# Kernel tuning notes

Hardware: AMD Instinct MI355X
Metric: run time of the kernel (lower is better)

The kernel has to match this reference:

```python
import jax, jax.numpy as jnp
import numpy as np
import math

B, S, SENC, D, H, FF, V = 4, 512, 512, 1024, 16, 4096, 50257
MAX_HOP = 6          # n_layers -> max ACT hops
THRESH = 1.0 - 0.01  # ACT halting threshold
EPS = 1e-12          # LAYER_NORM_EPS
NEG = -1e20          # neginf for fp32 masking
DH = D // H


def _sincos(n_pos, dim):
    # create_position_codes: sin on even dims, cos on odd dims
    pos = np.arange(n_pos, dtype=np.float64)[:, None]
    j = np.arange(dim // 2, dtype=np.float64)[None, :]
    ang = pos / np.power(10000.0, 2.0 * j / dim)
    out = np.zeros((n_pos, dim), dtype=np.float32)
    out[:, 0::2] = np.sin(ang)
    out[:, 1::2] = np.cos(ang)
    return jnp.asarray(out)


def setup_inputs() -> dict:
    key = jax.random.key(0)
    ks = jax.random.split(key, 20)
    def lin_w(k, fan_in, fan_out):
        return (jax.random.normal(k, (fan_in, fan_out), jnp.float32)
                * (1.0 / math.sqrt(fan_in)))
    inp = {
        "tokens": jax.random.randint(ks[0], (B, S), 0, V),
        "encoder_output": jax.random.normal(ks[1], (B, SENC, D), jnp.float32),
        "encoder_mask": jnp.ones((B, SENC), jnp.int32),
        "emb": jax.random.normal(ks[2], (V, D), jnp.float32) * 0.02,
        "sa_qw": lin_w(ks[3], D, D), "sa_qb": jnp.zeros((D,), jnp.float32),
        "sa_kw": lin_w(ks[4], D, D), "sa_kb": jnp.zeros((D,), jnp.float32),
        "sa_vw": lin_w(ks[5], D, D), "sa_vb": jnp.zeros((D,), jnp.float32),
        "sa_ow": lin_w(ks[6], D, D), "sa_ob": jnp.zeros((D,), jnp.float32),
        "ca_qw": lin_w(ks[7], D, D), "ca_qb": jnp.zeros((D,), jnp.float32),
        "ca_kw": lin_w(ks[8], D, D), "ca_kb": jnp.zeros((D,), jnp.float32),
        "ca_vw": lin_w(ks[9], D, D), "ca_vb": jnp.zeros((D,), jnp.float32),
        "ca_ow": lin_w(ks[10], D, D), "ca_ob": jnp.zeros((D,), jnp.float32),
        "ln1_g": jnp.ones((D,), jnp.float32), "ln1_b": jnp.zeros((D,), jnp.float32),
        "ln2_g": jnp.ones((D,), jnp.float32), "ln2_b": jnp.zeros((D,), jnp.float32),
        "ln3_g": jnp.ones((D,), jnp.float32), "ln3_b": jnp.zeros((D,), jnp.float32),
        "ff_w1": lin_w(ks[11], D, FF), "ff_b1": jnp.zeros((FF,), jnp.float32),
        "ff_w2": lin_w(ks[12], FF, D), "ff_b2": jnp.zeros((D,), jnp.float32),
        "act_w": jax.random.normal(ks[13], (D,), jnp.float32) * 0.02,
        "act_b": jnp.ones((), jnp.float32),  # p.bias.data.fill_(1)
    }
    return inp


def _ln(x, g, b):
    m = x.mean(-1, keepdims=True)
    v = ((x - m) ** 2).mean(-1, keepdims=True)
    return (x - m) / jnp.sqrt(v + EPS) * g + b


def _mha(x, kv, maskb, qw, qb, kw, kb, vw, vb, ow, ob):
    Bq, Sq, _ = x.shape
    Sk = kv.shape[1]
    q = (x @ qw + qb).reshape(Bq, Sq, H, DH).transpose(0, 2, 1, 3) / math.sqrt(DH)
    k = (kv @ kw + kb).reshape(Bq, Sk, H, DH).transpose(0, 2, 1, 3)
    v = (kv @ vw + vb).reshape(Bq, Sk, H, DH).transpose(0, 2, 1, 3)
    sc = jnp.einsum('bhqd,bhkd->bhqk', q, k)
    sc = jnp.where(maskb, sc, NEG)
    a = jax.nn.softmax(sc, axis=-1)
    o = jnp.einsum('bhqk,bhkd->bhqd', a, v).transpose(0, 2, 1, 3).reshape(Bq, Sq, D)
    return o @ ow + ob


def reference(tokens, encoder_output, encoder_mask, emb,
              sa_qw, sa_qb, sa_kw, sa_kb, sa_vw, sa_vb, sa_ow, sa_ob,
              ca_qw, ca_qb, ca_kw, ca_kb, ca_vw, ca_vb, ca_ow, ca_ob,
              ln1_g, ln1_b, ln2_g, ln2_b, ln3_g, ln3_b,
              ff_w1, ff_b1, ff_w2, ff_b2, act_w, act_b):
    pos_codes = _sincos(S, D)       # [S, D]
    time_codes = _sincos(MAX_HOP, D)  # [MAX_HOP, D]
    x = emb[tokens] * math.sqrt(D)  # embeddings_scale
    dec_mask = jnp.tril(jnp.ones((S, S), bool))[None, None]          # causal
    enc_maskb = (encoder_mask != 0)[:, None, None, :]                # [B,1,1,Senc]

    def layer(t):
        r = t
        t = _mha(t, t, dec_mask, sa_qw, sa_qb, sa_kw, sa_kb, sa_vw, sa_vb, sa_ow, sa_ob)
        t = _ln(t + r, ln1_g, ln1_b)
        r = t
        t = _mha(t, encoder_output, enc_maskb, ca_qw, ca_qb, ca_kw, ca_kb, ca_vw, ca_vb, ca_ow, ca_ob)
        t = _ln(t + r, ln2_g, ln2_b)
        r = t
        t = jax.nn.relu(t @ ff_w1 + ff_b1) @ ff_w2 + ff_b2
        return _ln(t + r, ln3_g, ln3_b)

    def step(carry, t_idx):
        tensor, prev, hp, rem, nup = carry
        tensor = tensor + pos_codes[None] + time_codes[t_idx][None, None]
        p = jax.nn.sigmoid(tensor @ act_w + act_b)                   # [B,S]
        still = (hp < 1.0).astype(jnp.float32)
        cond = hp + p * still
        new_halted = (cond > THRESH).astype(jnp.float32) * still
        still = (cond <= THRESH).astype(jnp.float32) * still
        hp = hp + p * still
        rem = rem + new_halted * (1.0 - hp)
        hp = hp + new_halted * rem
        nup = nup + still + new_halted
        uw = (p * still + new_halted * rem)[..., None]
        tensor = layer(tensor)
        prev = tensor * uw + prev * (1.0 - uw)
        return (tensor, prev, hp, rem, nup), None

    z = jnp.zeros((B, S), jnp.float32)
    init = (x, jnp.zeros_like(x), z, z, z)
    # Running all MAX_HOP steps is exactly equivalent to the torch while-loop:
    # after a position halts, its update weight is 0 and state is frozen.
    (_, prev, hp, rem, nup), _ = jax.lax.scan(step, init, jnp.arange(MAX_HOP))
    return prev
```

## Files before the change

kernel.cpp:

```cpp
#include <hip/hip_runtime.h>
#include <math.h>

#define BB 4
#define SS 512
#define SE 512
#define DD 1024
#define HH 16
#define FFD 4096
#define NHOP 6

typedef float f32x4 __attribute__((ext_vector_type(4)));
typedef _Float16 h8 __attribute__((ext_vector_type(8)));

#define GLD16(gp, lp)                                                     \
  __builtin_amdgcn_global_load_lds(                                       \
      (const __attribute__((address_space(1))) void*)(gp),                \
      (__attribute__((address_space(3))) void*)(lp), 16, 0, 0)

template <int N>
__device__ __forceinline__ void vwait() {
  if constexpr (N == 0) asm volatile("s_waitcnt vmcnt(0)" ::: "memory");
  else if constexpr (N == 4) asm volatile("s_waitcnt vmcnt(4)" ::: "memory");
  else if constexpr (N == 6) asm volatile("s_waitcnt vmcnt(6)" ::: "memory");
  else if constexpr (N == 8) asm volatile("s_waitcnt vmcnt(8)" ::: "memory");
}

__device__ __forceinline__ float blockSum256(float v, float* s4) {
#pragma unroll
  for (int m = 32; m >= 1; m >>= 1) v += __shfl_xor(v, m);
  __syncthreads();
  if ((threadIdx.x & 63) == 0) s4[threadIdx.x >> 6] = v;
  __syncthreads();
  return s4[0] + s4[1] + s4[2] + s4[3];
}

__device__ __forceinline__ void split16(float v, _Float16& h, _Float16& l) {
  h = (_Float16)v;
  l = (_Float16)(v - (float)h);
}

__device__ __forceinline__ int swzel(int row, int slot) {
  return (row << 6) + ((slot ^ (row & 7)) << 3);
}

__global__ void sincos_kernel(float* __restrict__ out, int n) {
  for (int i = blockIdx.x * blockDim.x + threadIdx.x; i < n;
       i += gridDim.x * blockDim.x) {
    int p = i >> 10, d = i & 1023, j = d >> 1;
    double ang = (double)p / pow(10000.0, (2.0 * j) / 1024.0);
    out[i] = (float)((d & 1) ? cos(ang) : sin(ang));
  }
}

__global__ void embed_kernel(const int* __restrict__ tok,
                             const float* __restrict__ emb,
                             float* __restrict__ out, int n) {
  for (int i = blockIdx.x * blockDim.x + threadIdx.x; i < n;
       i += gridDim.x * blockDim.x) {
    int row = i >> 10, d = i & 1023;
    out[i] = emb[(size_t)tok[row] * DD + d] * 32.0f;
  }
}

__global__ void asplit_kernel(const float* __restrict__ x,
                              _Float16* __restrict__ h,
                              _Float16* __restrict__ l, int n) {
  for (int i = blockIdx.x * blockDim.x + threadIdx.x; i < n;
       i += gridDim.x * blockDim.x)
    split16(x[i], h[i], l[i]);
}

__global__ void addcodes_kernel(_Float16* __restrict__ th,
                                _Float16* __restrict__ tl,
                                const float* __restrict__ ten,
                                const float* __restrict__ pos,
                                const float* __restrict__ tim, int hop, int n) {
  for (int i = blockIdx.x * blockDim.x + threadIdx.x; i < n;
       i += gridDim.x * blockDim.x) {
    int d = i & 1023, s = (i >> 10) & 511;
    float v = ten[i] + pos[(s << 10) | d] + tim[(hop << 10) | d];
    split16(v, th[i], tl[i]);
  }
}

__global__ __launch_bounds__(256)
void act_kernel(const _Float16* __restrict__ th, const _Float16* __restrict__ tl,
                const float* __restrict__ aw, const float* __restrict__ ab,
                float* __restrict__ hp, float* __restrict__ rem,
                float* __restrict__ uw) {
  __shared__ float s4[4];
  int row = blockIdx.x;
  size_t base = (size_t)row * DD;
  float s = 0.f;
#pragma unroll
  for (int k = 0; k < 4; ++k) {
    int d = threadIdx.x + k * 256;
    s += ((float)th[base + d] + (float)tl[base + d]) * aw[d];
  }
  float z = blockSum256(s, s4);
  if (threadIdx.x == 0) {
    z += ab[0];
    float p = 1.0f / (1.0f + expf(-z));
    float h = hp[row], rm = rem[row];
    float s0 = (h < 1.0f) ? 1.0f : 0.0f;
    float cond = h + p * s0;
    float nh = (cond > 0.99f) ? s0 : 0.0f;
    float s1 = (cond <= 0.99f) ? s0 : 0.0f;
    h = h + p * s1;
    rm = rm + nh * (1.0f - h);
    h = h + nh * rm;
    hp[row] = h;
    rem[row] = rm;
    uw[row] = p * s1 + nh * rm;
  }
}

__global__ __launch_bounds__(256)
void lnres_kernel(const float* __restrict__ a, const _Float16* __restrict__ rh,
                  const _Float16* __restrict__ rl, const float* __restrict__ g,
                  const float* __restrict__ be, float* __restrict__ outf,
                  _Float16* __restrict__ oh, _Float16* __restrict__ ol,
                  const float* __restrict__ uwv, float* __restrict__ po,
                  int mode) {
  __shared__ float s4[4];
  int row = blockIdx.x;
  size_t base = (size_t)row * DD;
  float x[4];
#pragma unroll
  for (int k = 0; k < 4; ++k) {
    size_t idx = base + threadIdx.x + k * 256;
    x[k] = a[idx] + ((float)rh[idx] + (float)rl[idx]);
  }
  float mean = blockSum256(x[0] + x[1] + x[2] + x[3], s4) * (1.0f / 1024.0f);
  float q = 0.f;
#pragma unroll
  for (int k = 0; k < 4; ++k) {
    float dv = x[k] - mean;
    q += dv * dv;
  }
  float var = blockSum256(q, s4) * (1.0f / 1024.0f);
  float inv = 1.0f / sqrtf(var + 1e-12f);
  float u = (mode == 0) ? uwv[row] : 0.f;
#pragma unroll
  for (int k = 0; k < 4; ++k) {
    int d = threadIdx.x + k * 256;
    size_t idx = base + d;
    float y = (x[k] - mean) * inv * g[d] + be[d];
    if (mode == 0) {
      outf[idx] = y;
      po[idx] = y * u + po[idx] * (1.0f - u);
    } else {
      split16(y, oh[idx], ol[idx]);
    }
  }
}

__global__ __launch_bounds__(256)
void wsplit_kernel(const float* __restrict__ W, _Float16* __restrict__ WhT,
                   _Float16* __restrict__ WlT, int K, int N) {
  __shared__ float t[32][33];
  int k0 = blockIdx.y << 5, n0 = blockIdx.x << 5;
  int c = threadIdx.x & 31, r8 = threadIdx.x >> 5;
  for (int rr = r8; rr < 32; rr += 8)
    t[rr][c] = W[(size_t)(k0 + rr) * N + n0 + c];
  __syncthreads();
  for (int rr = r8; rr < 32; rr += 8) {
    float v = t[c][rr];
    split16(v, WhT[(size_t)(n0 + rr) * K + k0 + c],
            WlT[(size_t)(n0 + rr) * K + k0 + c]);
  }
}

__global__ void concat3_kernel(const float* __restrict__ a,
                               const float* __restrict__ b,
                               const float* __restrict__ c,
                               float* __restrict__ o) {
  int i = blockIdx.x * 256 + threadIdx.x;
  if (i < 3072) o[i] = (i < 1024) ? a[i] : ((i < 2048) ? b[i - 1024] : c[i - 2048]);
}

__global__ __launch_bounds__(256)
void prep_vt_kernel(const float* __restrict__ src, int stride, int col0,
                    _Float16* __restrict__ oh, _Float16* __restrict__ ol) {
  __shared__ float t[64][65];
  int st = blockIdx.x;
  int bh = blockIdx.y;
  int b = bh >> 4, h = bh & 15;
  for (int kidx = threadIdx.x; kidx < 4096; kidx += 256) {
    int r = kidx >> 6, c = kidx & 63;
    t[r][c] = src[(size_t)(b * SS + st * 64 + r) * stride + col0 + h * 64 + c];
  }
  __syncthreads();
  for (int kidx = threadIdx.x; kidx < 4096; kidx += 256) {
    int d = kidx >> 6, s = kidx & 63;
    float v = t[s][d];
    size_t o = ((size_t)bh * 64 + d) * SS + st * 64 + s;
    split16(v, oh[o], ol[o]);
  }
}

template <int FM, int FN, int EPI>
__global__ __launch_bounds__(256) void gemm_pl(
    const _Float16* __restrict__ Ah, const _Float16* __restrict__ Al,
    const _Float16* __restrict__ Bh, const _Float16* __restrict__ Bl,
    const float* __restrict__ bias, float* __restrict__ Cf,
    _Float16* __restrict__ Ch, _Float16* __restrict__ Cl,
    _Float16* __restrict__ Ch2, _Float16* __restrict__ Cl2, int M, int N,
    int K, float scale) {
  constexpr int MT = FM * 32, NT = FN * 32;
  constexpr int SA = MT / 64;
  constexpr int SB = NT / 64;
  constexpr int L = 2 * (SA + SB);
  __shared__ __align__(16) _Float16 sA0[2][MT * 32], sA1[2][MT * 32];
  __shared__ __align__(16) _Float16 sB0[2][NT * 32], sB1[2][NT * 32];
  const int tid = threadIdx.x;
  const int lane = tid & 63, wid = tid >> 6;
  const int wr = wid >> 1, wc = wid & 1;
  int bx = blockIdx.x, by = blockIdx.y;
  {
    int nb = gridDim.x * gridDim.y;
    if ((nb & 7) == 0) {
      int flat = by * gridDim.x + bx;
      int swz = (flat & 7) * (nb >> 3) + (flat >> 3);
      bx = swz % gridDim.x;
      by = swz / gridDim.x;
    }
  }
  const int m0 = by * MT, n0 = bx * NT;
  const int l15 = lane & 15, l4 = lane >> 4;

  f32x4 acc[FM][FN];
#pragma unroll
  for (int i = 0; i < FM; ++i)
#pragma unroll
    for (int j = 0; j < FN; ++j) acc[i][j] = (f32x4){0.f, 0.f, 0.f, 0.f};

  auto STAGE = [&](int kt, int buf) {
    const int ko = kt << 5;
#pragma unroll
    for (int c = 0; c < SA; ++c) {
      int slot = tid + (c << 8);
      int row = slot >> 2, sl = slot & 3;
      int of = ((sl ^ ((row >> 1) & 3)) << 3);
      size_t ga = (size_t)(m0 + row) * K + ko + of;
      int de = (wid << 9) + (c << 11);
      GLD16(Ah + ga, &sA0[buf][de]);
      GLD16(Al + ga, &sA1[buf][de]);
    }
#pragma unroll
    for (int c = 0; c < SB; ++c) {
      int slot = tid + (c << 8);
      int row = slot >> 2, sl = slot & 3;
      int of = ((sl ^ ((row >> 1) & 3)) << 3);
      size_t ga = (size_t)(n0 + row) * K + ko + of;
      int de = (wid << 9) + (c << 11);
      GLD16(Bh + ga, &sB0[buf][de]);
      GLD16(Bl + ga, &sB1[buf][de]);
    }
  };

  const int nk = K >> 5;
  STAGE(0, 0);
  int cur = 0;
  for (int kt = 0; kt < nk; ++kt) {
    if (kt + 1 < nk) {
      STAGE(kt + 1, cur ^ 1);
      vwait<L>();
    } else {
      vwait<0>();
    }
    __builtin_amdgcn_s_barrier();
    __builtin_amdgcn_sched_barrier(0);
    const _Float16* pA0 = sA0[cur];
    const _Float16* pA1 = sA1[cur];
    const _Float16* pB0 = sB0[cur];
    const _Float16* pB1 = sB1[cur];
    h8 a0[FM], a1[FM], b0[FN], b1[FN];
#pragma unroll
    for (int f = 0; f < FM; ++f) {
      int m = wr * (FM * 16) + f * 16 + l15;
      int st = ((l4 ^ ((m >> 1) & 3)) << 3);
      a0[f] = *(const h8*)&pA0[(m << 5) + st];
      a1[f] = *(const h8*)&pA1[(m << 5) + st];
    }
#pragma unroll
    for (int f = 0; f < FN; ++f) {
      int n = wc * (FN * 16) + f * 16 + l15;
      int sn = ((l4 ^ ((n >> 1) & 3)) << 3);
      b0[f] = *(const h8*)&pB0[(n << 5) + sn];
      b1[f] = *(const h8*)&pB1[(n << 5) + sn];
    }
#pragma unroll
    for (int fi = 0; fi < FM; ++fi)
#pragma unroll
      for (int fj = 0; fj < FN; ++fj) {
        acc[fi][fj] = __builtin_amdgcn_mfma_f32_16x16x32_f16(
            a0[fi], b0[fj], acc[fi][fj], 0, 0, 0);
        acc[fi][fj] = __builtin_amdgcn_mfma_f32_16x16x32_f16(
            a1[fi], b0[fj], acc[fi][fj], 0, 0, 0);
        acc[fi][fj] = __builtin_amdgcn_mfma_f32_16x16x32_f16(
            a0[fi], b1[fj], acc[fi][fj], 0, 0, 0);
      }
    __builtin_amdgcn_sched_barrier(0);
    __builtin_amdgcn_s_barrier();
    cur ^= 1;
  }
#pragma unroll
  for (int fi = 0; fi < FM; ++fi) {
    int row = m0 + wr * (FM * 16) + fi * 16 + (l4 << 2);
#pragma unroll
    for (int fj = 0; fj < FN; ++fj) {
      int col = n0 + wc * (FN * 16) + fj * 16 + l15;
      float bz = bias[col];
#pragma unroll
      for (int r = 0; r < 4; ++r) {
        float o = acc[fi][fj][r] + bz;
        int rowr = row + r;
        if (EPI == 0) {
          Cf[(size_t)rowr * N + col] = o;
        } else if (EPI == 1) {
          o = fmaxf(o, 0.f);
          size_t idx = (size_t)rowr * N + col;
          split16(o, Ch[idx], Cl[idx]);
        } else if (EPI == 3) {
          o *= scale;
          int b = rowr >> 9, sr = rowr & 511, h = col >> 6, d = col & 63;
          size_t q = ((size_t)(b * HH + h) * SS + sr) * 64 + d;
          split16(o, Ch[q], Cl[q]);
        } else {
          int reg = col >> 10;
          int c = col & 1023;
          if (reg == 2) {
            Cf[(size_t)rowr * 1024 + c] = o;
          } else {
            if (reg == 0) o *= scale;
            int b = rowr >> 9, sr = rowr & 511, h = c >> 6, d = c & 63;
            size_t q = ((size_t)(b * HH + h) * SS + sr) * 64 + d;
            if (reg == 0) split16(o, Ch[q], Cl[q]);
            else split16(o, Ch2[q], Cl2[q]);
          }
        }
      }
    }
  }
}

template <int CAUSAL>
__global__ __launch_bounds__(256) void flash_mfma(
    const _Float16* __restrict__ Qph, const _Float16* __restrict__ Qpl,
    const _Float16* __restrict__ Kph, const _Float16* __restrict__ Kpl,
    const _Float16* __restrict__ Vph, const _Float16* __restrict__ Vpl,
    _Float16* __restrict__ AOh, _Float16* __restrict__ AOl,
    const int* __restrict__ mask, int Sk) {
  __shared__ __align__(16) _Float16 sKh[2][4096], sKl[2][4096];
  __shared__ __align__(16) _Float16 sVh[2][4096], sVl[2][4096];
  __shared__ __align__(16) _Float16 sPh[4096], sPl[4096];
  const int tid = threadIdx.x, lane = tid & 63, wid = tid >> 6;
  const int l15 = lane & 15, l4 = lane >> 4;
  const int flat = blockIdx.x;
  const int bh = flat >> 3, b = bh >> 4;
  int qt = flat & 7;
  if (CAUSAL && (flat >> 8)) qt = 7 - qt;
  const size_t qkb = (size_t)bh * SS * 64;
  const size_t vtb = (size_t)bh * 64 * Sk;

  int srow[2], slg[2], sde[2];
#pragma unroll
  for (int c = 0; c < 2; ++c) {
    int u = (c << 8) + tid;
    srow[c] = u >> 3;
    slg[c] = (u & 7) ^ (srow[c] & 7);
    sde[c] = (c << 11) + (wid << 9);
  }

  unsigned mbits = 0xFFFFFFFFu;
  if (!CAUSAL && mask != nullptr) {
    mbits = 0u;
#pragma unroll
    for (int kt = 0; kt < 8; ++kt)
#pragma unroll
      for (int fj = 0; fj < 4; ++fj)
        mbits |= (mask[b * Sk + kt * 64 + fj * 16 + l15] != 0 ? 1u : 0u)
                 << (kt * 4 + fj);
  }

  h8 aqh[2], aql[2];
#pragma unroll
  for (int ks = 0; ks < 2; ++ks) {
    size_t qa = qkb + (size_t)(qt * 64 + wid * 16 + l15) * 64 + ks * 32 + l4 * 8;
    aqh[ks] = *(const h8*)(Qph + qa);
    aql[ks] = *(const h8*)(Qpl + qa);
  }
  f32x4 o_[4];
  float m_[4], l_[4];
#pragma unroll
  for (int i = 0; i < 4; ++i) o_[i] = (f32x4){0.f, 0.f, 0.f, 0.f};
#pragma unroll
  for (int r = 0; r < 4; ++r) { m_[r] = -3.0e38f; l_[r] = 0.f; }

  auto STAGE = [&](int kt, int buf) {
#pragma unroll
    for (int c = 0; c < 2; ++c) {
      size_t ksrc = qkb + (size_t)(kt * 64 + srow[c]) * 64 + slg[c] * 8;
      size_t vsrc = vtb + (size_t)srow[c] * Sk + kt * 64 + slg[c] * 8;
      GLD16(Kph + ksrc, &sKh[buf][sde[c]]);
      GLD16(Kpl + ksrc, &sKl[buf][sde[c]]);
      GLD16(Vph + vsrc, &sVh[buf][sde[c]]);
      GLD16(Vpl + vsrc, &sVl[buf][sde[c]]);
    }
  };

  const int nkt = CAUSAL ? (qt + 1) : (Sk >> 6);
  STAGE(0, 0);
  int cur = 0;
  for (int kt = 0; kt < nkt; ++kt) {
    if (kt + 1 < nkt) {
      STAGE(kt + 1, cur ^ 1);
      vwait<8>();
    } else {
      vwait<0>();
    }
    __builtin_amdgcn_s_barrier();
    __builtin_amdgcn_sched_barrier(0);
    const _Float16* pKh = sKh[cur];
    const _Float16* pKl = sKl[cur];
    const _Float16* pVh = sVh[cur];
    const _Float16* pVl = sVl[cur];
    f32x4 sc[4];
#pragma unroll
    for (int fj = 0; fj < 4; ++fj) {
      sc[fj] = (f32x4){0.f, 0.f, 0.f, 0.f};
#pragma unroll
      for (int ks = 0; ks < 2; ++ks) {
        int off = swzel(fj * 16 + l15, ks * 4 + l4);
        h8 bkh = *(const h8*)&pKh[off];
        h8 bkl = *(const h8*)&pKl[off];
        sc[fj] = __builtin_amdgcn_mfma_f32_16x16x32_f16(aqh[ks], bkh, sc[fj], 0, 0, 0);
        sc[fj] = __builtin_amdgcn_mfma_f32_16x16x32_f16(aql[ks], bkh, sc[fj], 0, 0, 0);
        sc[fj] = __builtin_amdgcn_mfma_f32_16x16x32_f16(aqh[ks], bkl, sc[fj], 0, 0, 0);
      }
    }
    if (CAUSAL && kt == qt) {
#pragma unroll
      for (int fj = 0; fj < 4; ++fj)
#pragma unroll
        for (int r = 0; r < 4; ++r)
          if (fj * 16 + l15 > wid * 16 + l4 * 4 + r) sc[fj][r] = -1e20f;
    }
    if (!CAUSAL) {
#pragma unroll
      for (int fj = 0; fj < 4; ++fj)
        if (!((mbits >> (kt * 4 + fj)) & 1u)) {
#pragma unroll
          for (int r = 0; r < 4; ++r) sc[fj][r] = -1e20f;
        }
    }
#pragma unroll
    for (int r = 0; r < 4; ++r) {
      float rm = fmaxf(fmaxf(sc[0][r], sc[1][r]), fmaxf(sc[2][r], sc[3][r]));
#pragma unroll
      for (int mk = 1; mk < 16; mk <<= 1) rm = fmaxf(rm, __shfl_xor(rm, mk));
      float mn = fmaxf(m_[r], rm);
      float f = __expf(m_[r] - mn);
      float rs = 0.f;
      int prow = wid * 16 + l4 * 4 + r;
#pragma unroll
      for (int fj = 0; fj < 4; ++fj) {
        float p = __expf(sc[fj][r] - mn);
        rs += p;
        int col = fj * 16 + l15;
        int el = (prow << 6) + ((((col >> 3) ^ (prow & 7))) << 3) + (col & 7);
        _Float16 ph = (_Float16)p;
        sPh[el] = ph;
        sPl[el] = (_Float16)(p - (float)ph);
      }
#pragma unroll
      for (int mk = 1; mk < 16; mk <<= 1) rs += __shfl_xor(rs, mk);
      l_[r] = l_[r] * f + rs;
      m_[r] = mn;
#pragma unroll
      for (int df = 0; df < 4; ++df) o_[df][r] *= f;
    }
#pragma unroll
    for (int ks = 0; ks < 2; ++ks) {
      int poff = swzel(wid * 16 + l15, ks * 4 + l4);
      h8 aph = *(const h8*)&sPh[poff];
      h8 apl = *(const h8*)&sPl[poff];
#pragma unroll
      for (int df = 0; df < 4; ++df) {
        int voff = swzel(df * 16 + l15, ks * 4 + l4);
        h8 bvh = *(const h8*)&pVh[voff];
        h8 bvl = *(const h8*)&pVl[voff];
        o_[df] = __builtin_amdgcn_mfma_f32_16x16x32_f16(aph, bvh, o_[df], 0, 0, 0);
        o_[df] = __builtin_amdgcn_mfma_f32_16x16x32_f16(apl, bvh, o_[df], 0, 0, 0);
        o_[df] = __builtin_amdgcn_mfma_f32_16x16x32_f16(aph, bvl, o_[df], 0, 0, 0);
      }
    }
    __builtin_amdgcn_sched_barrier(0);
    __builtin_amdgcn_s_barrier();
    cur ^= 1;
  }
#pragma unroll
  for (int r = 0; r < 4; ++r) {
    float inv = 1.0f / l_[r];
    int row = qt * 64 + wid * 16 + l4 * 4 + r;
    size_t ob = ((size_t)b * SS + row) * DD + (bh & 15) * 64;
#pragma unroll
    for (int df = 0; df < 4; ++df) {
      float o = o_[df][r] * inv;
      split16(o, AOh[ob + df * 16 + l15], AOl[ob + df * 16 + l15]);
    }
  }
}

extern "C" void kernel_launch(void* const* d_in, const int* in_sizes, int n_in,
                              void* d_out, int out_size, void* d_ws,
                              size_t ws_size, hipStream_t stream) {
  const int* tokens = (const int*)d_in[0];
  const float* enc = (const float*)d_in[1];
  const int* encmask = (const int*)d_in[2];
  const float* emb = (const float*)d_in[3];
  const float* sa_qw = (const float*)d_in[4];
  const float* sa_qb = (const float*)d_in[5];
  const float* sa_kw = (const float*)d_in[6];
  const float* sa_kb = (const float*)d_in[7];
  const float* sa_vw = (const float*)d_in[8];
  const float* sa_vb = (const float*)d_in[9];
  const float* sa_ow = (const float*)d_in[10];
  const float* sa_ob = (const float*)d_in[11];
  const float* ca_qw = (const float*)d_in[12];
  const float* ca_qb = (const float*)d_in[13];
  const float* ca_kw = (const float*)d_in[14];
  const float* ca_kb = (const float*)d_in[15];
  const float* ca_vw = (const float*)d_in[16];
  const float* ca_vb = (const float*)d_in[17];
  const float* ca_ow = (const float*)d_in[18];
  const float* ca_ob = (const float*)d_in[19];
  const float* ln1_g = (const float*)d_in[20];
  const float* ln1_b = (const float*)d_in[21];
  const float* ln2_g = (const float*)d_in[22];
  const float* ln2_b = (const float*)d_in[23];
  const float* ln3_g = (const float*)d_in[24];
  const float* ln3_b = (const float*)d_in[25];
  const float* ff_w1 = (const float*)d_in[26];
  const float* ff_b1 = (const float*)d_in[27];
  const float* ff_w2 = (const float*)d_in[28];
  const float* ff_b2 = (const float*)d_in[29];
  const float* act_w = (const float*)d_in[30];
  const float* act_b = (const float*)d_in[31];
  float* out = (float*)d_out;

  const size_t nbsd = (size_t)BB * SS * DD;
  const size_t nff = (size_t)BB * SS * FFD;
  const size_t nbs = (size_t)BB * SS;
  const size_t wsm = (size_t)DD * DD;
  const size_t wff = (size_t)DD * FFD;

  float* w = (float*)d_ws;
  float* POS = w;  w += (size_t)SS * DD;
  float* TIM = w;  w += (size_t)NHOP * DD;
  float* TEN = w;  w += nbsd;
  float* PR = w;   w += nbsd;
  float* QKV = w;  w += (size_t)2048 * 3072;
  float* QKVB = w; w += 3072;
  float* HPp = w;  w += nbs;
  float* REMp = w; w += nbs;
  float* UWp = w;  w += nbs;
  _Float16* hp16 = (_Float16*)w;
  auto halloc = [&](size_t n) { _Float16* r = hp16; hp16 += n; return r; };
  _Float16* TINh = halloc(nbsd); _Float16* TINl = halloc(nbsd);
  _Float16* AOh = halloc(nbsd);  _Float16* AOl = halloc(nbsd);
  _Float16* FFHh = halloc(nff);  _Float16* FFHl = halloc(nff);
  _Float16* qkvWh = halloc(3 * wsm); _Float16* qkvWl = halloc(3 * wsm);
  _Float16* saoWh = halloc(wsm); _Float16* saoWl = halloc(wsm);
  _Float16* caqWh = halloc(wsm); _Float16* caqWl = halloc(wsm);
  _Float16* caoWh = halloc(wsm); _Float16* caoWl = halloc(wsm);
  _Float16* ff1Wh = halloc(wff); _Float16* ff1Wl = halloc(wff);
  _Float16* ff2Wh = halloc(wff); _Float16* ff2Wl = halloc(wff);
  _Float16* EKh = halloc(nbsd); _Float16* EKl = halloc(nbsd);
  _Float16* EVh = halloc(nbsd); _Float16* EVl = halloc(nbsd);
  size_t need = (size_t)((char*)hp16 - (char*)d_ws);
  if (ws_size < need) return;

  float* VF32 = QKV;
  _Float16* T3h = TINh; _Float16* T3l = TINl;
  _Float16* T2h = (_Float16*)(QKV + nbsd);
  _Float16* T2l = (_Float16*)(QKV + nbsd + nbsd / 2);
  _Float16* Qph = FFHh;             _Float16* Qpl = FFHh + nbsd;
  _Float16* Kph = FFHh + 2 * nbsd;  _Float16* Kpl = FFHh + 3 * nbsd;
  _Float16* Vph = FFHl;             _Float16* Vpl = FFHl + nbsd;
  _Float16* CQh = FFHl + 2 * nbsd;  _Float16* CQl = FFHl + 3 * nbsd;

  hipMemsetAsync(d_out, 0, nbsd * sizeof(float), stream);
  hipMemsetAsync(HPp, 0, 2 * nbs * sizeof(float), stream);
  sincos_kernel<<<dim3(512), dim3(256), 0, stream>>>(POS, SS * DD);
  sincos_kernel<<<dim3(24), dim3(256), 0, stream>>>(TIM, NHOP * DD);
  embed_kernel<<<dim3(2048), dim3(256), 0, stream>>>(tokens, emb, TEN, (int)nbsd);
  asplit_kernel<<<dim3(2048), dim3(256), 0, stream>>>(enc, TINh, TINl, (int)nbsd);

  auto wsplit = [&](const float* W, _Float16* h, _Float16* l, int K, int N) {
    wsplit_kernel<<<dim3(N >> 5, K >> 5), dim3(256), 0, stream>>>(W, h, l, K, N);
  };
  wsplit(sa_qw, qkvWh, qkvWl, DD, DD);
  wsplit(sa_kw, qkvWh + wsm, qkvWl + wsm, DD, DD);
  wsplit(sa_vw, qkvWh + 2 * wsm, qkvWl + 2 * wsm, DD, DD);
  wsplit(sa_ow, saoWh, saoWl, DD, DD);
  wsplit(ca_qw, caqWh, caqWl, DD, DD);
  wsplit(ca_kw, FFHh, FFHh + wsm, DD, DD);
  wsplit(ca_vw, FFHh + 2 * wsm, FFHh + 3 * wsm, DD, DD);
  wsplit(ca_ow, caoWh, caoWl, DD, DD);
  wsplit(ff_w1, ff1Wh, ff1Wl, DD, FFD);
  wsplit(ff_w2, ff2Wh, ff2Wl, FFD, DD);
  concat3_kernel<<<dim3(12), dim3(256), 0, stream>>>(sa_qb, sa_kb, sa_vb, QKVB);

  auto gemmF = [&](const _Float16* ah, const _Float16* al, const _Float16* bh,
                   const _Float16* bl, const float* bi, float* cf, int M, int N,
                   int K) {
    gemm_pl<2, 2, 0><<<dim3(N / 64, M / 64), dim3(256), 0, stream>>>(
        ah, al, bh, bl, bi, cf, nullptr, nullptr, nullptr, nullptr, M, N, K,
        1.f);
  };

  gemm_pl<2, 2, 3><<<dim3(16, 32), dim3(256), 0, stream>>>(
      TINh, TINl, FFHh, FFHh + wsm, ca_kb, nullptr, EKh, EKl, nullptr, nullptr,
      2048, DD, DD, 1.f);
  gemmF(TINh, TINl, FFHh + 2 * wsm, FFHh + 3 * wsm, ca_vb, VF32, 2048, DD, DD);
  prep_vt_kernel<<<dim3(8, 64), dim3(256), 0, stream>>>(VF32, DD, 0, EVh, EVl);

  for (int t = 0; t < NHOP; ++t) {
    addcodes_kernel<<<dim3(2048), dim3(256), 0, stream>>>(TINh, TINl, TEN, POS,
                                                          TIM, t, (int)nbsd);
    act_kernel<<<dim3(2048), dim3(256), 0, stream>>>(TINh, TINl, act_w, act_b,
                                                     HPp, REMp, UWp);
    gemm_pl<4, 2, 2><<<dim3(48, 16), dim3(256), 0, stream>>>(
        TINh, TINl, qkvWh, qkvWl, QKVB, VF32, Qph, Qpl, Kph, Kpl, 2048, 3072,
        DD, 0.125f);
    prep_vt_kernel<<<dim3(8, 64), dim3(256), 0, stream>>>(VF32, DD, 0, Vph, Vpl);
    flash_mfma<1><<<dim3(512), dim3(256), 0, stream>>>(
        Qph, Qpl, Kph, Kpl, Vph, Vpl, AOh, AOl, nullptr, SS);
    gemmF(AOh, AOl, saoWh, saoWl, sa_ob, PR, 2048, DD, DD);
    lnres_kernel<<<dim3(2048), dim3(256), 0, stream>>>(
        PR, TINh, TINl, ln1_g, ln1_b, nullptr, T2h, T2l, nullptr, nullptr, 1);
    gemm_pl<2, 2, 3><<<dim3(16, 32), dim3(256), 0, stream>>>(
        T2h, T2l, caqWh, caqWl, ca_qb, nullptr, CQh, CQl, nullptr, nullptr,
        2048, DD, DD, 0.125f);
    flash_mfma<0><<<dim3(512), dim3(256), 0, stream>>>(
        CQh, CQl, EKh, EKl, EVh, EVl, AOh, AOl, encmask, SE);
    gemmF(AOh, AOl, caoWh, caoWl, ca_ob, PR, 2048, DD, DD);
    lnres_kernel<<<dim3(2048), dim3(256), 0, stream>>>(
        PR, T2h, T2l, ln2_g, ln2_b, nullptr, T3h, T3l, nullptr, nullptr, 1);
    gemm_pl<4, 2, 1><<<dim3(64, 16), dim3(256), 0, stream>>>(
        T3h, T3l, ff1Wh, ff1Wl, ff_b1, nullptr, FFHh, FFHl, nullptr, nullptr,
        2048, FFD, DD, 1.f);
    gemmF(FFHh, FFHl, ff2Wh, ff2Wl, ff_b2, PR, 2048, DD, FFD);
    lnres_kernel<<<dim3(2048), dim3(256), 0, stream>>>(
        PR, T3h, T3l, ln3_g, ln3_b, TEN, nullptr, nullptr, UWp, out, 0);
  }
}
```

Before: 2.321 ms.

## Fuse code-add with ACT, write V transposed from GEMM epilogue, use K=64 tiles

Merges the position/time code addition into the ACT halting kernel, so the hop input is read once and the dot product uses the exact fp32 value. The V projection (self and cross attention) now writes its transposed fp16 hi/lo layout straight from the GEMM epilogue, which removes the fp32 intermediate and the separate prep_vt transpose kernels. The GEMM is fixed at a 64x64 tile with a 64-wide K step and a new swizzle, replacing the 128x64 tiles used for QKV and FF1. Smaller tiles double the grid for those GEMMs but cut operand reuse per block.

```diff
diff --git a/kernel.cpp b/kernel.cpp
--- a/kernel.cpp
+++ b/kernel.cpp
@@ -11,6 +11,7 @@
 
 typedef float f32x4 __attribute__((ext_vector_type(4)));
 typedef _Float16 h8 __attribute__((ext_vector_type(8)));
+typedef _Float16 h4 __attribute__((ext_vector_type(4)));
 
 #define GLD16(gp, lp)                                                     \
   __builtin_amdgcn_global_load_lds(                                       \
@@ -20,8 +21,6 @@
 template <int N>
 __device__ __forceinline__ void vwait() {
   if constexpr (N == 0) asm volatile("s_waitcnt vmcnt(0)" ::: "memory");
-  else if constexpr (N == 4) asm volatile("s_waitcnt vmcnt(4)" ::: "memory");
-  else if constexpr (N == 6) asm volatile("s_waitcnt vmcnt(6)" ::: "memory");
   else if constexpr (N == 8) asm volatile("s_waitcnt vmcnt(8)" ::: "memory");
 }
 
@@ -70,32 +69,24 @@
     split16(x[i], h[i], l[i]);
 }
 
-__global__ void addcodes_kernel(_Float16* __restrict__ th,
-                                _Float16* __restrict__ tl,
-                                const float* __restrict__ ten,
-                                const float* __restrict__ pos,
-                                const float* __restrict__ tim, int hop, int n) {
-  for (int i = blockIdx.x * blockDim.x + threadIdx.x; i < n;
-       i += gridDim.x * blockDim.x) {
-    int d = i & 1023, s = (i >> 10) & 511;
-    float v = ten[i] + pos[(s << 10) | d] + tim[(hop << 10) | d];
-    split16(v, th[i], tl[i]);
-  }
-}
-
 __global__ __launch_bounds__(256)
-void act_kernel(const _Float16* __restrict__ th, const _Float16* __restrict__ tl,
-                const float* __restrict__ aw, const float* __restrict__ ab,
-                float* __restrict__ hp, float* __restrict__ rem,
-                float* __restrict__ uw) {
+void actcodes_kernel(const float* __restrict__ ten, const float* __restrict__ pos,
+                     const float* __restrict__ tim, int hop,
+                     const float* __restrict__ aw, const float* __restrict__ ab,
+                     float* __restrict__ hp, float* __restrict__ rem,
+                     float* __restrict__ uw, _Float16* __restrict__ th,
+                     _Float16* __restrict__ tl) {
   __shared__ float s4[4];
   int row = blockIdx.x;
+  int srow = row & 511;
   size_t base = (size_t)row * DD;
   float s = 0.f;
 #pragma unroll
   for (int k = 0; k < 4; ++k) {
     int d = threadIdx.x + k * 256;
-    s += ((float)th[base + d] + (float)tl[base + d]) * aw[d];
+    float v = ten[base + d] + pos[(srow << 10) + d] + tim[(hop << 10) + d];
+    split16(v, th[base + d], tl[base + d]);
+    s += v * aw[d];
   }
   float z = blockSum256(s, s4);
   if (threadIdx.x == 0) {
@@ -179,40 +170,17 @@
   if (i < 3072) o[i] = (i < 1024) ? a[i] : ((i < 2048) ? b[i - 1024] : c[i - 2048]);
 }
 
-__global__ __launch_bounds__(256)
-void prep_vt_kernel(const float* __restrict__ src, int stride, int col0,
-                    _Float16* __restrict__ oh, _Float16* __restrict__ ol) {
-  __shared__ float t[64][65];
-  int st = blockIdx.x;
-  int bh = blockIdx.y;
-  int b = bh >> 4, h = bh & 15;
-  for (int kidx = threadIdx.x; kidx < 4096; kidx += 256) {
-    int r = kidx >> 6, c = kidx & 63;
-    t[r][c] = src[(size_t)(b * SS + st * 64 + r) * stride + col0 + h * 64 + c];
-  }
-  __syncthreads();
-  for (int kidx = threadIdx.x; kidx < 4096; kidx += 256) {
-    int d = kidx >> 6, s = kidx & 63;
-    float v = t[s][d];
-    size_t o = ((size_t)bh * 64 + d) * SS + st * 64 + s;
-    split16(v, oh[o], ol[o]);
-  }
-}
-
-template <int FM, int FN, int EPI>
+template <int EPI>
 __global__ __launch_bounds__(256) void gemm_pl(
     const _Float16* __restrict__ Ah, const _Float16* __restrict__ Al,
     const _Float16* __restrict__ Bh, const _Float16* __restrict__ Bl,
     const float* __restrict__ bias, float* __restrict__ Cf,
     _Float16* __restrict__ Ch, _Float16* __restrict__ Cl,
-    _Float16* __restrict__ Ch2, _Float16* __restrict__ Cl2, int M, int N,
+    _Float16* __restrict__ Ch2, _Float16* __restrict__ Cl2,
+    _Float16* __restrict__ Ch3, _Float16* __restrict__ Cl3, int M, int N,
     int K, float scale) {
-  constexpr int MT = FM * 32, NT = FN * 32;
-  constexpr int SA = MT / 64;
-  constexpr int SB = NT / 64;
-  constexpr int L = 2 * (SA + SB);
-  __shared__ __align__(16) _Float16 sA0[2][MT * 32], sA1[2][MT * 32];
-  __shared__ __align__(16) _Float16 sB0[2][NT * 32], sB1[2][NT * 32];
+  __shared__ __align__(16) _Float16 sA0[2][4096], sA1[2][4096];
+  __shared__ __align__(16) _Float16 sB0[2][4096], sB1[2][4096];
   const int tid = threadIdx.x;
   const int lane = tid & 63, wid = tid >> 6;
   const int wr = wid >> 1, wc = wid & 1;
@@ -226,46 +194,38 @@
       by = swz / gridDim.x;
     }
   }
-  const int m0 = by * MT, n0 = bx * NT;
+  const int m0 = by << 6, n0 = bx << 6;
   const int l15 = lane & 15, l4 = lane >> 4;
 
-  f32x4 acc[FM][FN];
-#pragma unroll
-  for (int i = 0; i < FM; ++i)
-#pragma unroll
-    for (int j = 0; j < FN; ++j) acc[i][j] = (f32x4){0.f, 0.f, 0.f, 0.f};
+  f32x4 acc[2][2];
+#pragma unroll
+  for (int i = 0; i < 2; ++i)
+#pragma unroll
+    for (int j = 0; j < 2; ++j) acc[i][j] = (f32x4){0.f, 0.f, 0.f, 0.f};
 
   auto STAGE = [&](int kt, int buf) {
-    const int ko = kt << 5;
-#pragma unroll
-    for (int c = 0; c < SA; ++c) {
-      int slot = tid + (c << 8);
-      int row = slot >> 2, sl = slot & 3;
-      int of = ((sl ^ ((row >> 1) & 3)) << 3);
-      size_t ga = (size_t)(m0 + row) * K + ko + of;
-      int de = (wid << 9) + (c << 11);
+    const int ko = kt << 6;
+#pragma unroll
+    for (int c = 0; c < 2; ++c) {
+      int idx = (c << 8) + tid;
+      int row = idx >> 3, gs = (idx & 7) ^ (row & 7);
+      int de = (c << 11) + (wid << 9);
+      size_t ga = (size_t)(m0 + row) * K + ko + (gs << 3);
       GLD16(Ah + ga, &sA0[buf][de]);
       GLD16(Al + ga, &sA1[buf][de]);
-    }
-#pragma unroll
-    for (int c = 0; c < SB; ++c) {
-      int slot = tid + (c << 8);
-      int row = slot >> 2, sl = slot & 3;
-      int of = ((sl ^ ((row >> 1) & 3)) << 3);
-      size_t ga = (size_t)(n0 + row) * K + ko + of;
-      int de = (wid << 9) + (c << 11);
-      GLD16(Bh + ga, &sB0[buf][de]);
-      GLD16(Bl + ga, &sB1[buf][de]);
+      size_t gb = (size_t)(n0 + row) * K + ko + (gs << 3);
+      GLD16(Bh + gb, &sB0[buf][de]);
+      GLD16(Bl + gb, &sB1[buf][de]);
     }
   };
 
-  const int nk = K >> 5;
+  const int nk = K >> 6;
   STAGE(0, 0);
   int cur = 0;
   for (int kt = 0; kt < nk; ++kt) {
     if (kt + 1 < nk) {
       STAGE(kt + 1, cur ^ 1);
-      vwait<L>();
+      vwait<8>();
     } else {
       vwait<0>();
     }
@@ -275,66 +235,99 @@
     const _Float16* pA1 = sA1[cur];
     const _Float16* pB0 = sB0[cur];
     const _Float16* pB1 = sB1[cur];
-    h8 a0[FM], a1[FM], b0[FN], b1[FN];
-#pragma unroll
-    for (int f = 0; f < FM; ++f) {
-      int m = wr * (FM * 16) + f * 16 + l15;
-      int st = ((l4 ^ ((m >> 1) & 3)) << 3);
-      a0[f] = *(const h8*)&pA0[(m << 5) + st];
-      a1[f] = *(const h8*)&pA1[(m << 5) + st];
-    }
-#pragma unroll
-    for (int f = 0; f < FN; ++f) {
-      int n = wc * (FN * 16) + f * 16 + l15;
-      int sn = ((l4 ^ ((n >> 1) & 3)) << 3);
-      b0[f] = *(const h8*)&pB0[(n << 5) + sn];
-      b1[f] = *(const h8*)&pB1[(n << 5) + sn];
-    }
-#pragma unroll
-    for (int fi = 0; fi < FM; ++fi)
-#pragma unroll
-      for (int fj = 0; fj < FN; ++fj) {
-        acc[fi][fj] = __builtin_amdgcn_mfma_f32_16x16x32_f16(
-            a0[fi], b0[fj], acc[fi][fj], 0, 0, 0);
-        acc[fi][fj] = __builtin_amdgcn_mfma_f32_16x16x32_f16(
-            a1[fi], b0[fj], acc[fi][fj], 0, 0, 0);
-        acc[fi][fj] = __builtin_amdgcn_mfma_f32_16x16x32_f16(
-            a0[fi], b1[fj], acc[fi][fj], 0, 0, 0);
+#pragma unroll
+    for (int ks = 0; ks < 2; ++ks) {
+      h8 a0[2], a1[2], b0[2], b1[2];
+#pragma unroll
+      for (int f = 0; f < 2; ++f) {
+        int m = (wr << 5) + (f << 4) + l15;
+        int so = swzel(m, (ks << 2) + l4);
+        a0[f] = *(const h8*)&pA0[so];
+        a1[f] = *(const h8*)&pA1[so];
+        int n = (wc << 5) + (f << 4) + l15;
+        int sn = swzel(n, (ks << 2) + l4);
+        b0[f] = *(const h8*)&pB0[sn];
+        b1[f] = *(const h8*)&pB1[sn];
       }
+#pragma unroll
+      for (int fi = 0; fi < 2; ++fi)
+#pragma unroll
+        for (int fj = 0; fj < 2; ++fj) {
+          acc[fi][fj] = __builtin_amdgcn_mfma_f32_16x16x32_f16(
+              a0[fi], b0[fj], acc[fi][fj], 0, 0, 0);
+          acc[fi][fj] = __builtin_amdgcn_mfma_f32_16x16x32_f16(
+              a1[fi], b0[fj], acc[fi][fj], 0, 0, 0);
+          acc[fi][fj] = __builtin_amdgcn_mfma_f32_16x16x32_f16(
+              a0[fi], b1[fj], acc[fi][fj], 0, 0, 0);
+        }
+    }
     __builtin_amdgcn_sched_barrier(0);
     __builtin_amdgcn_s_barrier();
     cur ^= 1;
   }
 #pragma unroll
-  for (int fi = 0; fi < FM; ++fi) {
-    int row = m0 + wr * (FM * 16) + fi * 16 + (l4 << 2);
-#pragma unroll
-    for (int fj = 0; fj < FN; ++fj) {
-      int col = n0 + wc * (FN * 16) + fj * 16 + l15;
+  for (int fi = 0; fi < 2; ++fi) {
+    int row = m0 + (wr << 5) + (fi << 4) + (l4 << 2);
+#pragma unroll
+    for (int fj = 0; fj < 2; ++fj) {
+      int col = n0 + (wc << 5) + (fj << 4) + l15;
       float bz = bias[col];
-#pragma unroll
-      for (int r = 0; r < 4; ++r) {
-        float o = acc[fi][fj][r] + bz;
-        int rowr = row + r;
-        if (EPI == 0) {
-          Cf[(size_t)rowr * N + col] = o;
-        } else if (EPI == 1) {
-          o = fmaxf(o, 0.f);
-          size_t idx = (size_t)rowr * N + col;
+      float ov[4];
+#pragma unroll
+      for (int r = 0; r < 4; ++r) ov[r] = acc[fi][fj][r] + bz;
+      if (EPI == 0) {
+#pragma unroll
+        for (int r = 0; r < 4; ++r) Cf[(size_t)(row + r) * N + col] = ov[r];
+      } else if (EPI == 1) {
+#pragma unroll
+        for (int r = 0; r < 4; ++r) {
+          float o = fmaxf(ov[r], 0.f);
+          size_t idx = (size_t)(row + r) * N + col;
           split16(o, Ch[idx], Cl[idx]);
-        } else if (EPI == 3) {
-          o *= scale;
-          int b = rowr >> 9, sr = rowr & 511, h = col >> 6, d = col & 63;
+        }
+      } else if (EPI == 3) {
+        int b = row >> 9, h = col >> 6, d = col & 63;
+#pragma unroll
+        for (int r = 0; r < 4; ++r) {
+          int sr = (row + r) & 511;
           size_t q = ((size_t)(b * HH + h) * SS + sr) * 64 + d;
-          split16(o, Ch[q], Cl[q]);
+          split16(ov[r] * scale, Ch[q], Cl[q]);
+        }
+      } else if (EPI == 4) {
+        int b = row >> 9, s0 = row & 511, h = col >> 6, d = col & 63;
+        h4 hv, lv;
+#pragma unroll
+        for (int r = 0; r < 4; ++r) {
+          _Float16 hh, ll;
+          split16(ov[r], hh, ll);
+          hv[r] = hh;
+          lv[r] = ll;
+        }
+        size_t vo = ((size_t)(b * HH + h) * 64 + d) * SS + s0;
+        *(h4*)&Ch[vo] = hv;
+        *(h4*)&Cl[vo] = lv;
+      } else {
+        int reg = col >> 10;
+        int c = col & 1023;
+        int b = row >> 9, h = c >> 6, d = c & 63;
+        if (reg == 2) {
+          int s0 = row & 511;
+          h4 hv, lv;
+#pragma unroll
+          for (int r = 0; r < 4; ++r) {
+            _Float16 hh, ll;
+            split16(ov[r], hh, ll);
+            hv[r] = hh;
+            lv[r] = ll;
+          }
+          size_t vo = ((size_t)(b * HH + h) * 64 + d) * SS + s0;
+          *(h4*)&Ch3[vo] = hv;
+          *(h4*)&Cl3[vo] = lv;
         } else {
-          int reg = col >> 10;
-          int c = col & 1023;
-          if (reg == 2) {
-            Cf[(size_t)rowr * 1024 + c] = o;
-          } else {
-            if (reg == 0) o *= scale;
-            int b = rowr >> 9, sr = rowr & 511, h = c >> 6, d = c & 63;
+#pragma unroll
+          for (int r = 0; r < 4; ++r) {
+            float o = (reg == 0) ? ov[r] * scale : ov[r];
+            int sr = (row + r) & 511;
             size_t q = ((size_t)(b * HH + h) * SS + sr) * 64 + d;
             if (reg == 0) split16(o, Ch[q], Cl[q]);
             else split16(o, Ch2[q], Cl2[q]);
@@ -561,7 +554,7 @@
   float* TIM = w;  w += (size_t)NHOP * DD;
   float* TEN = w;  w += nbsd;
   float* PR = w;   w += nbsd;
-  float* QKV = w;  w += (size_t)2048 * 3072;
+  float* T2R = w;  w += (size_t)2048 * 3072;
   float* QKVB = w; w += 3072;
   float* HPp = w;  w += nbs;
   float* REMp = w; w += nbs;
@@ -582,10 +575,9 @@
   size_t need = (size_t)((char*)hp16 - (char*)d_ws);
   if (ws_size < need) return;
 
-  float* VF32 = QKV;
   _Float16* T3h = TINh; _Float16* T3l = TINl;
-  _Float16* T2h = (_Float16*)(QKV + nbsd);
-  _Float16* T2l = (_Float16*)(QKV + nbsd + nbsd / 2);
+  _Float16* T2h = (_Float16*)T2R;
+  _Float16* T2l = (_Float16*)T2R + nbsd;
   _Float16* Qph = FFHh;             _Float16* Qpl = FFHh + nbsd;
   _Float16* Kph = FFHh + 2 * nbsd;  _Float16* Kpl = FFHh + 3 * nbsd;
   _Float16* Vph = FFHl;             _Float16* Vpl = FFHl + nbsd;
@@ -616,42 +608,40 @@
   auto gemmF = [&](const _Float16* ah, const _Float16* al, const _Float16* bh,
                    const _Float16* bl, const float* bi, float* cf, int M, int N,
                    int K) {
-    gemm_pl<2, 2, 0><<<dim3(N / 64, M / 64), dim3(256), 0, stream>>>(
-        ah, al, bh, bl, bi, cf, nullptr, nullptr, nullptr, nullptr, M, N, K,
-        1.f);
+    gemm_pl<0><<<dim3(N / 64, M / 64), dim3(256), 0, stream>>>(
+        ah, al, bh, bl, bi, cf, nullptr, nullptr, nullptr, nullptr, nullptr,
+        nullptr, M, N, K, 1.f);
   };
 
-  gemm_pl<2, 2, 3><<<dim3(16, 32), dim3(256), 0, stream>>>(
+  gemm_pl<3><<<dim3(16, 32), dim3(256), 0, stream>>>(
       TINh, TINl, FFHh, FFHh + wsm, ca_kb, nullptr, EKh, EKl, nullptr, nullptr,
-      2048, DD, DD, 1.f);
-  gemmF(TINh, TINl, FFHh + 2 * wsm, FFHh + 3 * wsm, ca_vb, VF32, 2048, DD, DD);
-  prep_vt_kernel<<<dim3(8, 64), dim3(256), 0, stream>>>(VF32, DD, 0, EVh, EVl);
+      nullptr, nullptr, 2048, DD, DD, 1.f);
+  gemm_pl<4><<<dim3(16, 32), dim3(256), 0, stream>>>(
+      TINh, TINl, FFHh + 2 * wsm, FFHh + 3 * wsm, ca_vb, nullptr, EVh, EVl,
+      nullptr, nullptr, nullptr, nullptr, 2048, DD, DD, 1.f);
 
   for (int t = 0; t < NHOP; ++t) {
-    addcodes_kernel<<<dim3(2048), dim3(256), 0, stream>>>(TINh, TINl, TEN, POS,
-                                                          TIM, t, (int)nbsd);
-    act_kernel<<<dim3(2048), dim3(256), 0, stream>>>(TINh, TINl, act_w, act_b,
-                                                     HPp, REMp, UWp);
-    gemm_pl<4, 2, 2><<<dim3(48, 16), dim3(256), 0, stream>>>(
-        TINh, TINl, qkvWh, qkvWl, QKVB, VF32, Qph, Qpl, Kph, Kpl, 2048, 3072,
-        DD, 0.125f);
-    prep_vt_kernel<<<dim3(8, 64), dim3(256), 0, stream>>>(VF32, DD, 0, Vph, Vpl);
+    actcodes_kernel<<<dim3(2048), dim3(256), 0, stream>>>(
+        TEN, POS, TIM, t, act_w, act_b, HPp, REMp, UWp, TINh, TINl);
+    gemm_pl<2><<<dim3(48, 32), dim3(256), 0, stream>>>(
+        TINh, TINl, qkvWh, qkvWl, QKVB, nullptr, Qph, Qpl, Kph, Kpl, Vph, Vpl,
+        2048, 3072, DD, 0.125f);
     flash_mfma<1><<<dim3(512), dim3(256), 0, stream>>>(
         Qph, Qpl, Kph, Kpl, Vph, Vpl, AOh, AOl, nullptr, SS);
     gemmF(AOh, AOl, saoWh, saoWl, sa_ob, PR, 2048, DD, DD);
     lnres_kernel<<<dim3(2048), dim3(256), 0, stream>>>(
         PR, TINh, TINl, ln1_g, ln1_b, nullptr, T2h, T2l, nullptr, nullptr, 1);
-    gemm_pl<2, 2, 3><<<dim3(16, 32), dim3(256), 0, stream>>>(
+    gemm_pl<3><<<dim3(16, 32), dim3(256), 0, stream>>>(
         T2h, T2l, caqWh, caqWl, ca_qb, nullptr, CQh, CQl, nullptr, nullptr,
-        2048, DD, DD, 0.125f);
+        nullptr, nullptr, 2048, DD, DD, 0.125f);
     flash_mfma<0><<<dim3(512), dim3(256), 0, stream>>>(
         CQh, CQl, EKh, EKl, EVh, EVl, AOh, AOl, encmask, SE);
     gemmF(AOh, AOl, caoWh, caoWl, ca_ob, PR, 2048, DD, DD);
     lnres_kernel<<<dim3(2048), dim3(256), 0, stream>>>(
         PR, T2h, T2l, ln2_g, ln2_b, nullptr, T3h, T3l, nullptr, nullptr, 1);
-    gemm_pl<4, 2, 1><<<dim3(64, 16), dim3(256), 0, stream>>>(
+    gemm_pl<1><<<dim3(64, 32), dim3(256), 0, stream>>>(
         T3h, T3l, ff1Wh, ff1Wl, ff_b1, nullptr, FFHh, FFHl, nullptr, nullptr,
-        2048, FFD, DD, 1.f);
+        nullptr, nullptr, 2048, FFD, DD, 1.f);
     gemmF(FFHh, FFHl, ff2Wh, ff2Wl, ff_b2, PR, 2048, DD, FFD);
     lnres_kernel<<<dim3(2048), dim3(256), 0, stream>>>(
         PR, T3h, T3l, ln3_g, ln3_b, TEN, nullptr, nullptr, UWp, out, 0);
```

Result: faster. 2.165 ms (-6.7%).
